# Kernel tuning notes

Measured on AMD Instinct MI355X. Metric: run time of the kernel, lower is better.

Reference implementation:

```python
import jax, jax.numpy as jnp
import numpy as np

EPS = 1e-5
NUM_GROUPS = 32
NUM_HEADS = 8

def group_norm(x, w, b):
    # x: (B, C, H, W), 32 groups, affine per-channel
    B, C, H, W = x.shape
    xg = x.reshape(B, NUM_GROUPS, C // NUM_GROUPS, H, W)
    mu = xg.mean(axis=(2, 3, 4), keepdims=True)
    var = xg.var(axis=(2, 3, 4), keepdims=True)
    xn = ((xg - mu) * jax.lax.rsqrt(var + EPS)).reshape(B, C, H, W)
    return xn * w[None, :, None, None] + b[None, :, None, None]

def conv1x1(x, w, b):
    # 1x1 conv == per-pixel linear; w: (out, in), x: (B, C, H, W)
    return jnp.einsum('oc,bchw->bohw', w, x) + b[None, :, None, None]

def setup_inputs() -> dict:
    key = jax.random.key(0)
    ks = jax.random.split(key, 4)
    B, C, H, W = 2, 512, 64, 64
    s = 1.0 / np.sqrt(C)
    return {
        'x': jax.random.normal(ks[0], (B, C, H, W), jnp.float32),
        'gn_w': jnp.ones((C,), jnp.float32),
        'gn_b': jnp.zeros((C,), jnp.float32),
        'wq': jax.random.normal(ks[1], (C, C), jnp.float32) * s,
        'bq': jnp.zeros((C,), jnp.float32),
        'wkv': jax.random.normal(ks[2], (2 * C, C), jnp.float32) * s,
        'bkv': jnp.zeros((2 * C,), jnp.float32),
        'wo': jax.random.normal(ks[3], (C, C), jnp.float32) * s,
        'bo': jnp.zeros((C,), jnp.float32),
    }

def reference(x, gn_w, gn_b, wq, bq, wkv, bkv, wo, bo):
    B, C, H, W = x.shape
    hd = C // NUM_HEADS  # head_dim
    residual = x
    x_norm = group_norm(x, gn_w, gn_b)
    q = conv1x1(x_norm, wq, bq).reshape(B, NUM_HEADS, hd, H * W)
    kv = conv1x1(x_norm, wkv, bkv)
    k, v = jnp.split(kv, 2, axis=1)
    k = k.reshape(B, NUM_HEADS, hd, H * W)
    v = v.reshape(B, NUM_HEADS, hd, H * W)
    scale = hd ** (-0.5)
    attn = jnp.einsum('bhdi,bhdj->bhij', q, k) * scale
    attn = jax.nn.softmax(attn, axis=-1)
    out = jnp.einsum('bhij,bhdj->bhdi', attn, v).reshape(B, C, H, W)
    out = conv1x1(out, wo, bo)
    return out + residual
```

## Files before the change

kernel.cpp:

```cpp
#include <hip/hip_runtime.h>
#include <cmath>

typedef __bf16 bf16x8 __attribute__((ext_vector_type(8)));
typedef __bf16 bf16x4 __attribute__((ext_vector_type(4)));
typedef float  f32x4  __attribute__((ext_vector_type(4)));
typedef unsigned uint2_ev __attribute__((ext_vector_type(2)));

static __device__ __forceinline__ f32x4 mfma16(bf16x8 a, bf16x8 b, f32x4 c) {
    return __builtin_amdgcn_mfma_f32_16x16x32_bf16(a, b, c, 0, 0, 0);
}

static __device__ __forceinline__ float fast_exp2(float x) {
#if __has_builtin(__builtin_amdgcn_exp2f)
    return __builtin_amdgcn_exp2f(x);
#else
    return exp2f(x);
#endif
}

static __device__ __forceinline__ void quad_swap(unsigned &a, unsigned &b) {
#if __has_builtin(__builtin_amdgcn_permlane32_swap) && __has_builtin(__builtin_amdgcn_permlane16_swap)
    uint2_ev r32 = __builtin_amdgcn_permlane32_swap(a, b, false, false);
    uint2_ev r16 = __builtin_amdgcn_permlane16_swap(r32[0], r32[1], false, false);
    a = r16[0]; b = r16[1];
#else
    asm volatile("v_permlane32_swap_b32 %0, %1\n\t"
                 "v_permlane16_swap_b32 %0, %1"
                 : "+v"(a), "+v"(b));
#endif
}

static __device__ __forceinline__ void gload_lds16(const void* g, void* l) {
    __builtin_amdgcn_global_load_lds((const __attribute__((address_space(1))) void*)g,
                                     (__attribute__((address_space(3))) void*)l, 16, 0, 0);
}

#define OFF_STATS 0
#define OFF_BEFF  1024
#define OFF_W     16384
#define OFF_XNT   (4u*1024*1024)
#define OFF_QKT   (OFF_XNT + 8u*1024*1024)
#define OFF_V     (OFF_QKT + 16u*1024*1024)
#define OFF_OP    (OFF_V + 8u*1024*1024)
#define CHUNK_O   4194304u
#define CHUNK_L   65536u

__global__ __launch_bounds__(256) void gn_fuse(const float* __restrict__ x,
                                               float* __restrict__ stats,
                                               __bf16* __restrict__ xT) {
    int p0 = blockIdx.x * 64, c0 = blockIdx.y * 64, b = blockIdx.z;
    int tid = threadIdx.x, lane = tid & 63, wave = tid >> 6;
    __shared__ float t[64][68];
    __shared__ float red[4][8];
    float acc_s[4] = {0.f,0.f,0.f,0.f}, acc_ss[4] = {0.f,0.f,0.f,0.f};
    const int rr = tid >> 4;
    const int p4 = (tid & 15) * 4;
    #pragma unroll
    for (int i = 0; i < 4; ++i) {
        int cc = rr + 16*i;
        float4 v = *(const float4*)&x[((size_t)(b*512 + c0 + cc) << 12) + p0 + p4];
        *(float4*)&t[cc][p4] = v;
        acc_s[i]  += v.x + v.y + v.z + v.w;
        acc_ss[i] += v.x*v.x + v.y*v.y + v.z*v.z + v.w*v.w;
    }
    #pragma unroll
    for (int g = 0; g < 4; ++g) {
        #pragma unroll
        for (int off = 1; off < 64; off <<= 1) {
            acc_s[g]  += __shfl_xor(acc_s[g],  off);
            acc_ss[g] += __shfl_xor(acc_ss[g], off);
        }
    }
    if (lane == 0) {
        #pragma unroll
        for (int g = 0; g < 4; ++g) { red[wave][g*2] = acc_s[g]; red[wave][g*2+1] = acc_ss[g]; }
    }
    __syncthreads();
    if (tid < 8) {
        float v0 = red[0][tid] + red[1][tid] + red[2][tid] + red[3][tid];
        int g = (b << 5) + (c0 >> 4) + (tid >> 1);
        atomicAdd(&stats[g*2 + (tid & 1)], v0);
    }
    const int ch = tid & 7;
    #pragma unroll
    for (int w = 0; w < 2; ++w) {
        int pp = (tid >> 3) + 32*w;
        __bf16 ob[8];
        #pragma unroll
        for (int e = 0; e < 8; ++e) ob[e] = (__bf16)t[ch*8 + e][pp];
        *(bf16x8*)&xT[((size_t)(b*4096 + p0 + pp) << 9) + c0 + ch*8] = *(bf16x8*)ob;
    }
}

__global__ __launch_bounds__(256) void prep_w(const float* __restrict__ wq,
                                              const float* __restrict__ wkv,
                                              const float* __restrict__ wo,
                                              const float* __restrict__ bq,
                                              const float* __restrict__ bkv,
                                              const float* __restrict__ stats,
                                              const float* __restrict__ gw,
                                              const float* __restrict__ gb,
                                              __bf16* __restrict__ wS,
                                              __bf16* __restrict__ wo_bf,
                                              float* __restrict__ beff) {
    const int b = blockIdx.y, bx = blockIdx.x;
    const int tid = threadIdx.x, lane = tid & 63, wave = tid >> 6;
    if (bx >= 48) {
        if (b) return;
        int r0 = (bx - 48) * 32;
        #pragma unroll
        for (int ps = 0; ps < 8; ++ps) {
            int row = r0 + ps*4 + wave;
            __bf16 obuf[8];
            #pragma unroll
            for (int e = 0; e < 8; ++e) obuf[e] = (__bf16)wo[(size_t)row*512 + lane*8 + e];
            *(bf16x8*)&wo_bf[(size_t)row*512 + lane*8] = *(bf16x8*)obuf;
        }
        return;
    }
    __shared__ float sS[512], sT[512];
    for (int c = tid; c < 512; c += 256) {
        int g = (b << 5) + (c >> 4);
        float mu   = stats[g*2] * (1.f/65536.f);
        float var  = stats[g*2+1] * (1.f/65536.f) - mu*mu;
        float rstd = rsqrtf(var + 1e-5f);
        float s = rstd * gw[c];
        sS[c] = s;
        sT[c] = gb[c] - mu * s;
    }
    __syncthreads();
    int r0 = bx * 32;
    #pragma unroll
    for (int ps = 0; ps < 8; ++ps) {
        int row = r0 + ps*4 + wave;
        const float* Wrow = (row < 512) ? (wq + (size_t)row*512) : (wkv + (size_t)(row-512)*512);
        float bias0 = (row < 512) ? bq[row] : bkv[row - 512];
        float bp = 0.f;
        __bf16 obuf[8];
        #pragma unroll
        for (int e = 0; e < 8; ++e) {
            int c = lane*8 + e;
            float wv_ = Wrow[c];
            obuf[e] = (__bf16)(wv_ * sS[c]);
            bp += wv_ * sT[c];
        }
        *(bf16x8*)&wS[((size_t)b*1536 + row)*512 + lane*8] = *(bf16x8*)obuf;
        #pragma unroll
        for (int off = 1; off < 64; off <<= 1) bp += __shfl_xor(bp, off);
        if (lane == 0) beff[b*1536 + row] = bias0 + bp;
    }
}

__global__ __launch_bounds__(256) void gemm128_kernel(
    const __bf16* __restrict__ A, const __bf16* __restrict__ B,
    const float* __restrict__ bias, int nsplit,
    float scale0, void* __restrict__ out,
    int N, int K, long long strideA, long long strideB, long long strideO, int biasStride) {
    const int bz = blockIdx.z;
    A += strideA * bz;
    B += strideB * bz;
    const float* bb = bias + (size_t)bz * biasStride;
    const int m0 = blockIdx.x * 128, n0 = blockIdx.y * 128;
    const int tid = threadIdx.x, lane = tid & 63, wave = tid >> 6;
    const int quad = lane >> 4, l16 = lane & 15;
    const int wm = (wave >> 1) * 64, wn = (wave & 1) * 64;

    __shared__ __attribute__((aligned(16))) __bf16 lds_a[2][128][64];
    __shared__ __attribute__((aligned(16))) __bf16 lds_b[2][128][64];

    f32x4 acc[4][4];
    #pragma unroll
    for (int mt = 0; mt < 4; ++mt)
        #pragma unroll
        for (int nt = 0; nt < 4; ++nt)
            #pragma unroll
            for (int r = 0; r < 4; ++r) acc[mt][nt][r] = 0.f;

    const int myrow = (wave << 3) + (lane >> 3);
    const int mych  = ((lane & 7) ^ (myrow & 7)) << 3;
    const __bf16* Ab = A + (size_t)(m0 + myrow) * K + mych;
    const __bf16* Bb = B + (size_t)(n0 + myrow) * K + mych;

    auto stage = [&](int buf, int kt) {
        char* la = (char*)(&lds_a[buf][0][0]) + (wave << 10);
        char* lb = (char*)(&lds_b[buf][0][0]) + (wave << 10);
        #pragma unroll
        for (int i = 0; i < 4; ++i) {
            gload_lds16(Ab + kt + (size_t)(32*i) * K, la + i*4096);
            gload_lds16(Bb + kt + (size_t)(32*i) * K, lb + i*4096);
        }
    };

    stage(0, 0);
    const int NK = K >> 6;
    for (int k8 = 0; k8 < NK; ++k8) {
        __syncthreads();
        const int cur = k8 & 1;
        if (k8 + 1 < NK) stage(cur ^ 1, (k8 + 1) << 6);
        #pragma unroll
        for (int kh = 0; kh < 2; ++kh) {
            bf16x8 af[4], bfr[4];
            #pragma unroll
            for (int mt = 0; mt < 4; ++mt)
                af[mt] = *(const bf16x8*)&lds_a[cur][wm + mt*16 + l16][(((kh<<2)|quad) ^ (l16 & 7)) * 8];
            #pragma unroll
            for (int nt = 0; nt < 4; ++nt)
                bfr[nt] = *(const bf16x8*)&lds_b[cur][wn + nt*16 + l16][(((kh<<2)|quad) ^ (l16 & 7)) * 8];
            #pragma unroll
            for (int mt = 0; mt < 4; ++mt)
                #pragma unroll
                for (int nt = 0; nt < 4; ++nt)
                    acc[mt][nt] = mfma16(af[mt], bfr[nt], acc[mt][nt]);
        }
    }

    #pragma unroll
    for (int mt = 0; mt < 4; ++mt) {
        const int mrow = m0 + wm + mt*16 + quad*4;
        #pragma unroll
        for (int nt = 0; nt < 4; ++nt) {
            const int ncol = n0 + wn + nt*16 + l16;
            #pragma unroll
            for (int r = 0; r < 4; ++r) {
                const int m = mrow + r;
                float val = acc[mt][nt][r] + bb[ncol];
                if (ncol < nsplit) val *= scale0;
                ((__bf16*)out)[(size_t)strideO * bz + (size_t)m * N + ncol] = (__bf16)val;
            }
        }
    }
}

template<int OUT_F32, int HAS_RES>
__global__ __launch_bounds__(256) void gemm64_kernel(
    const __bf16* __restrict__ A, const __bf16* __restrict__ B,
    const float* __restrict__ bias, const float* __restrict__ res,
    void* __restrict__ out,
    int N, int K, long long strideA, long long strideB, long long strideO, int biasStride) {
    const int bz = blockIdx.z;
    A += strideA * bz;
    B += strideB * bz;
    const float* bb = bias + (size_t)bz * biasStride;
    const int m0 = blockIdx.x * 64, n0 = blockIdx.y * 128;
    const int tid = threadIdx.x, lane = tid & 63, wave = tid >> 6;
    const int quad = lane >> 4, l16 = lane & 15;
    const int wn = wave * 32;

    __shared__ __attribute__((aligned(16))) __bf16 lds_a[2][64][64];
    __shared__ __attribute__((aligned(16))) __bf16 lds_b[2][128][64];

    f32x4 acc[4][2];
    #pragma unroll
    for (int mt = 0; mt < 4; ++mt)
        #pragma unroll
        for (int nt = 0; nt < 2; ++nt)
            #pragma unroll
            for (int r = 0; r < 4; ++r) acc[mt][nt][r] = 0.f;

    const int myrow = (wave << 3) + (lane >> 3);
    const int mych  = ((lane & 7) ^ (myrow & 7)) << 3;
    const __bf16* Ab = A + (size_t)(m0 + myrow) * K + mych;
    const __bf16* Bb = B + (size_t)(n0 + myrow) * K + mych;

    auto stage = [&](int buf, int kt) {
        char* la = (char*)(&lds_a[buf][0][0]) + (wave << 10);
        char* lb = (char*)(&lds_b[buf][0][0]) + (wave << 10);
        #pragma unroll
        for (int i = 0; i < 2; ++i)
            gload_lds16(Ab + kt + (size_t)(32*i) * K, la + i*4096);
        #pragma unroll
        for (int i = 0; i < 4; ++i)
            gload_lds16(Bb + kt + (size_t)(32*i) * K, lb + i*4096);
    };

    stage(0, 0);
    const int NK = K >> 6;
    for (int k8 = 0; k8 < NK; ++k8) {
        __syncthreads();
        const int cur = k8 & 1;
        if (k8 + 1 < NK) stage(cur ^ 1, (k8 + 1) << 6);
        #pragma unroll
        for (int kh = 0; kh < 2; ++kh) {
            bf16x8 af[4], bfr[2];
            #pragma unroll
            for (int mt = 0; mt < 4; ++mt)
                af[mt] = *(const bf16x8*)&lds_a[cur][mt*16 + l16][(((kh<<2)|quad) ^ (l16 & 7)) * 8];
            #pragma unroll
            for (int nt = 0; nt < 2; ++nt)
                bfr[nt] = *(const bf16x8*)&lds_b[cur][wn + nt*16 + l16][(((kh<<2)|quad) ^ (l16 & 7)) * 8];
            #pragma unroll
            for (int mt = 0; mt < 4; ++mt)
                #pragma unroll
                for (int nt = 0; nt < 2; ++nt)
                    acc[mt][nt] = mfma16(af[mt], bfr[nt], acc[mt][nt]);
        }
    }

    #pragma unroll
    for (int mt = 0; mt < 4; ++mt) {
        const int mrow = m0 + mt*16 + quad*4;
        #pragma unroll
        for (int nt = 0; nt < 2; ++nt) {
            const int ncol = n0 + wn + nt*16 + l16;
            #pragma unroll
            for (int r = 0; r < 4; ++r) {
                const int m = mrow + r;
                float val = acc[mt][nt][r] + bb[m];
                const size_t idx = (size_t)strideO * bz + (size_t)m * N + ncol;
                if constexpr (HAS_RES) val += res[idx];
                if constexpr (OUT_F32) ((float*)out)[idx] = val;
                else ((__bf16*)out)[idx] = (__bf16)val;
            }
        }
    }
}

template<int NCH>
__global__ __launch_bounds__(256, 3) void attn_kernel(const __bf16* __restrict__ qkT,
                                                      const __bf16* __restrict__ v,
                                                      __bf16* __restrict__ attnT,
                                                      __bf16* __restrict__ Opart,
                                                      float* __restrict__ Lpart) {
    const int b = blockIdx.y >> 3, h = blockIdx.y & 7;
    const int chunk = (NCH > 1) ? blockIdx.z : 0;
    int NITER, kt0;
    if constexpr (NCH == 3) {
        NITER = (chunk == 0) ? 22 : 21;
        kt0   = (chunk == 0) ? 0 : (chunk == 1 ? 1408 : 2752);
    } else {
        NITER = 64 / NCH;
        kt0   = chunk * (4096 / NCH);
    }
    const int tid = threadIdx.x;
    const int wave = tid >> 6, lane = tid & 63;
    const int quad = lane >> 4, l16 = lane & 15;
    const int qbase = blockIdx.x * 256 + wave * 64;

    const __bf16* qkTb = qkT + ((size_t)b << 22);
    const __bf16* vb   = v   + ((size_t)b << 21);

    __shared__ __attribute__((aligned(16))) __bf16 lds_k[2][64][64];
    __shared__ __attribute__((aligned(16))) __bf16 lds_v[2][64][64];

    bf16x8 aq[4][2];
    #pragma unroll
    for (int mt = 0; mt < 4; ++mt) {
        const __bf16* qrow = qkTb + (size_t)(qbase + mt*16 + l16) * 1024 + h*64 + quad*8;
        aq[mt][0] = *(const bf16x8*)qrow;
        aq[mt][1] = *(const bf16x8*)(qrow + 32);
    }
    f32x4 o[4][5];
    #pragma unroll
    for (int mt = 0; mt < 4; ++mt)
        #pragma unroll
        for (int dt = 0; dt < 5; ++dt)
            #pragma unroll
            for (int r = 0; r < 4; ++r) o[mt][dt][r] = 0.f;
    const f32x4 kZero = {0.f, 0.f, 0.f, 0.f};

    bf16x8 onesb;
    #pragma unroll
    for (int e = 0; e < 8; ++e) onesb[e] = (__bf16)1.0f;

    const int myrow = (wave << 3) + (lane >> 3);
    const int mych  = ((lane & 7) ^ (myrow & 7)) << 3;
    const __bf16* kgb = qkTb + (size_t)myrow * 1024 + 512 + h*64 + mych;
    const __bf16* vgb = vb + ((size_t)(h*64 + myrow) << 12) + mych;

    auto stage = [&](int buf, int kt) {
        char* kb = (char*)(&lds_k[buf][0][0]) + (wave << 10);
        char* vp = (char*)(&lds_v[buf][0][0]) + (wave << 10);
        const __bf16* kg = kgb + (size_t)kt * 1024;
        const __bf16* vg = vgb + kt;
        gload_lds16(kg,                       kb);
        gload_lds16(kg + 32*1024,             kb + 4096);
        gload_lds16(vg,                       vp);
        gload_lds16(vg + ((size_t)32 << 12),  vp + 4096);
    };

    stage(0, kt0);

    for (int it = 0; it < NITER; ++it) {
        __syncthreads();
        const int cur = it & 1;
        if (it + 1 < NITER) stage(cur ^ 1, kt0 + (it + 1) * 64);

        #pragma unroll
        for (int kh = 0; kh < 2; ++kh) {
            __builtin_amdgcn_s_setprio(1);
            unsigned pd[4][4];
            #pragma unroll
            for (int j = 0; j < 2; ++j) {
                const int nt = kh*2 + j;
                const int kr = nt*16 + l16;
                bf16x8 bk0 = *(const bf16x8*)&lds_k[cur][kr][( quad      ^ (l16 & 7)) * 8];
                bf16x8 bk1 = *(const bf16x8*)&lds_k[cur][kr][((4 + quad) ^ (l16 & 7)) * 8];
                #pragma unroll
                for (int mt = 0; mt < 4; ++mt) {
                    f32x4 s = mfma16(bk1, aq[mt][1], mfma16(bk0, aq[mt][0], kZero));
                    f32x4 p;
                    #pragma unroll
                    for (int r = 0; r < 4; ++r) p[r] = fast_exp2(s[r]);
                    bf16x4 pb = __builtin_convertvector(p, bf16x4);
                    union { bf16x4 v; unsigned d[2]; } u; u.v = pb;
                    pd[mt][j*2]     = u.d[0];
                    pd[mt][j*2 + 1] = u.d[1];
                }
            }
            bf16x8 pa[4];
            #pragma unroll
            for (int mt = 0; mt < 4; ++mt) {
                unsigned x0 = pd[mt][0], x1 = pd[mt][1];
                unsigned y0 = pd[mt][2], y1 = pd[mt][3];
                quad_swap(x0, y0);
                quad_swap(x1, y1);
                union { unsigned d[4]; bf16x8 v; } u;
                u.d[0] = x0; u.d[1] = x1; u.d[2] = y0; u.d[3] = y1;
                pa[mt] = u.v;
            }
            #pragma unroll
            for (int dt = 0; dt < 4; ++dt) {
                bf16x8 bv = *(const bf16x8*)&lds_v[cur][dt*16 + l16][((kh*4 + quad) ^ (l16 & 7)) * 8];
                #pragma unroll
                for (int mt = 0; mt < 4; ++mt)
                    o[mt][dt] = mfma16(pa[mt], bv, o[mt][dt]);
            }
            #pragma unroll
            for (int mt = 0; mt < 4; ++mt)
                o[mt][4] = mfma16(pa[mt], onesb, o[mt][4]);
            __builtin_amdgcn_s_setprio(0);
        }
    }

    if constexpr (NCH > 1) {
        __bf16* Ob = Opart + (size_t)chunk * CHUNK_O;
        #pragma unroll
        for (int mt = 0; mt < 4; ++mt)
            #pragma unroll
            for (int dt = 0; dt < 4; ++dt)
                #pragma unroll
                for (int r = 0; r < 4; ++r) {
                    size_t row = (size_t)b * 4096 + qbase + mt*16 + quad*4 + r;
                    Ob[(row << 9) + (h << 6) + dt*16 + l16] = (__bf16)o[mt][dt][r];
                }
        if (l16 == 0) {
            #pragma unroll
            for (int mt = 0; mt < 4; ++mt)
                #pragma unroll
                for (int r = 0; r < 4; ++r) {
                    int p = qbase + mt*16 + quad*4 + r;
                    Lpart[(size_t)chunk * CHUNK_L + (size_t)(((b*8 + h)) << 12) + p] = o[mt][4][r];
                }
        }
    } else {
        #pragma unroll
        for (int mt = 0; mt < 4; ++mt) {
            float inv[4];
            #pragma unroll
            for (int r = 0; r < 4; ++r)
                inv[r] = 1.f / __shfl(o[mt][4][r], lane & 48);
            #pragma unroll
            for (int dt = 0; dt < 4; ++dt)
                #pragma unroll
                for (int r = 0; r < 4; ++r) {
                    size_t row = (size_t)b * 4096 + qbase + mt*16 + quad*4 + r;
                    attnT[(row << 9) + (h << 6) + dt*16 + l16] = (__bf16)(o[mt][dt][r] * inv[r]);
                }
        }
    }
}

template<int NCH>
__global__ __launch_bounds__(256) void attn_combine(const __bf16* __restrict__ Opart,
                                                    const float* __restrict__ Lpart,
                                                    __bf16* __restrict__ attnT) {
    int i = blockIdx.x * 256 + threadIdx.x;
    int c8 = i & 63;
    int p  = (i >> 6) & 4095;
    int b  = i >> 18;
    int h  = c8 >> 3;
    size_t lidx = (size_t)((b*8 + h) << 12) + p;
    float l = 0.f;
    #pragma unroll
    for (int ch = 0; ch < NCH; ++ch) l += Lpart[(size_t)ch * CHUNK_L + lidx];
    float inv = 1.f / l;
    size_t oi = ((size_t)(b*4096 + p) << 9) + c8*8;
    float acc[8] = {0.f,0.f,0.f,0.f,0.f,0.f,0.f,0.f};
    #pragma unroll
    for (int ch = 0; ch < NCH; ++ch) {
        bf16x8 ov = *(const bf16x8*)&Opart[(size_t)ch * CHUNK_O + oi];
        #pragma unroll
        for (int r = 0; r < 8; ++r) acc[r] += (float)ov[r];
    }
    bf16x8 rv;
    #pragma unroll
    for (int r = 0; r < 8; ++r) rv[r] = (__bf16)(acc[r] * inv);
    *(bf16x8*)&attnT[oi] = rv;
}

extern "C" void kernel_launch(void* const* d_in, const int* in_sizes, int n_in,
                              void* d_out, int out_size, void* d_ws, size_t ws_size,
                              hipStream_t stream) {
    const float* x   = (const float*)d_in[0];
    const float* gnw = (const float*)d_in[1];
    const float* gnb = (const float*)d_in[2];
    const float* wq  = (const float*)d_in[3];
    const float* bq  = (const float*)d_in[4];
    const float* wkv = (const float*)d_in[5];
    const float* bkv = (const float*)d_in[6];
    const float* wo  = (const float*)d_in[7];
    const float* bo  = (const float*)d_in[8];
    float* out = (float*)d_out;

    char* ws = (char*)d_ws;
    float*  stats  = (float*)(ws + OFF_STATS);
    float*  beff   = (float*)(ws + OFF_BEFF);
    __bf16* wS     = (__bf16*)(ws + OFF_W);
    __bf16* wo_bf  = wS + 2u*1536*512;
    __bf16* xT     = (__bf16*)(ws + OFF_XNT);
    __bf16* qkT    = (__bf16*)(ws + OFF_QKT);
    __bf16* vv     = (__bf16*)(ws + OFF_V);
    __bf16* Opart  = (__bf16*)(ws + OFF_OP);
    __bf16* attnT  = xT;

    const size_t need3 = (size_t)OFF_OP + 3u * (CHUNK_O * 2 + CHUNK_L * 4);
    const size_t need2 = (size_t)OFF_OP + 2u * (CHUNK_O * 2 + CHUNK_L * 4);
    const int nch = (ws_size >= need3) ? 3 : (ws_size >= need2 ? 2 : 1);
    float* Lpart = (float*)(ws + OFF_OP + (size_t)nch * CHUNK_O * 2);

    hipMemsetAsync(stats, 0, 512, stream);
    gn_fuse<<<dim3(64, 8, 2), 256, 0, stream>>>(x, stats, xT);
    prep_w<<<dim3(64, 2), 256, 0, stream>>>(wq, wkv, wo, bq, bkv, stats, gnw, gnb,
                                            wS, wo_bf, beff);

    const long long S  = 2097152LL;
    const long long S2 = 4194304LL;
    const long long SW = 1536LL*512;
    gemm128_kernel<<<dim3(32, 8, 2), 256, 0, stream>>>(
        xT, wS, beff, 512, 0.125f * 1.44269504f, qkT, 1024, 512, S, SW, S2, 1536);
    gemm64_kernel<0,0><<<dim3(8, 32, 2), 256, 0, stream>>>(
        wS + 1024*512, xT, beff + 1024, nullptr, vv, 4096, 512, SW, S, S, 1536);

    if (nch == 3) {
        attn_kernel<3><<<dim3(16, 16, 3), 256, 0, stream>>>(qkT, vv, nullptr, Opart, Lpart);
        attn_combine<3><<<2048, 256, 0, stream>>>(Opart, Lpart, attnT);
    } else if (nch == 2) {
        attn_kernel<2><<<dim3(16, 16, 2), 256, 0, stream>>>(qkT, vv, nullptr, Opart, Lpart);
        attn_combine<2><<<2048, 256, 0, stream>>>(Opart, Lpart, attnT);
    } else {
        attn_kernel<1><<<dim3(16, 16, 1), 256, 0, stream>>>(qkT, vv, attnT, nullptr, nullptr);
    }

    gemm64_kernel<1,1><<<dim3(8, 32, 2), 256, 0, stream>>>(
        wo_bf, attnT, bo, x, out, 4096, 512, 0, S, S, 0);
}
```

Before: 214.0 us.

## Fuse attention split-combine into output projection GEMM B-operand loading

Removes the separate attn_combine kernel and instead sums the partial attention outputs and normalizes by the summed softmax denominators while staging the B tile of the output-projection GEMM. This avoids a launch and the write/read round trip of the combined attention tensor. In exchange, B staging switches from direct global-to-LDS loads to register loads plus arithmetic and LDS stores, and each m-block re-reads all chunk partials.

```diff
diff --git a/kernel.cpp b/kernel.cpp
--- a/kernel.cpp
+++ b/kernel.cpp
@@ -231,10 +231,11 @@
     }
 }
 
-template<int OUT_F32, int HAS_RES>
+template<int OUT_F32, int HAS_RES, int COMB>
 __global__ __launch_bounds__(256) void gemm64_kernel(
     const __bf16* __restrict__ A, const __bf16* __restrict__ B,
     const float* __restrict__ bias, const float* __restrict__ res,
+    const float* __restrict__ Lp,
     void* __restrict__ out,
     int N, int K, long long strideA, long long strideB, long long strideO, int biasStride) {
     const int bz = blockIdx.z;
@@ -262,23 +263,71 @@
     const __bf16* Ab = A + (size_t)(m0 + myrow) * K + mych;
     const __bf16* Bb = B + (size_t)(n0 + myrow) * K + mych;
 
-    auto stage = [&](int buf, int kt) {
+    auto stageA = [&](int buf, int kt) {
         char* la = (char*)(&lds_a[buf][0][0]) + (wave << 10);
-        char* lb = (char*)(&lds_b[buf][0][0]) + (wave << 10);
         #pragma unroll
         for (int i = 0; i < 2; ++i)
             gload_lds16(Ab + kt + (size_t)(32*i) * K, la + i*4096);
+    };
+    auto stageB_dma = [&](int buf, int kt) {
+        char* lb = (char*)(&lds_b[buf][0][0]) + (wave << 10);
         #pragma unroll
         for (int i = 0; i < 4; ++i)
             gload_lds16(Bb + kt + (size_t)(32*i) * K, lb + i*4096);
     };
 
-    stage(0, 0);
+    bf16x8 brq[4][COMB ? COMB : 1];
+    float  lq [4][COMB ? COMB : 1];
+    auto loadB = [&](int kt) {
+        if constexpr (COMB) {
+            const int h = kt >> 6;
+            #pragma unroll
+            for (int i = 0; i < 4; ++i) {
+                const int p = n0 + myrow + 32*i;
+                const size_t bi = (((size_t)bz*4096 + p) << 9) + kt + mych;
+                const size_t li = ((size_t)((bz*8 + h)) << 12) + p;
+                #pragma unroll
+                for (int ch = 0; ch < COMB; ++ch) {
+                    brq[i][ch] = *(const bf16x8*)&B[(size_t)ch * CHUNK_O + bi];
+                    lq[i][ch]  = Lp[(size_t)ch * CHUNK_L + li];
+                }
+            }
+        }
+    };
+    auto writeB = [&](int buf) {
+        if constexpr (COMB) {
+            #pragma unroll
+            for (int i = 0; i < 4; ++i) {
+                float l = 0.f;
+                #pragma unroll
+                for (int ch = 0; ch < COMB; ++ch) l += lq[i][ch];
+                float inv = 1.f / l;
+                __bf16 ob[8];
+                #pragma unroll
+                for (int e = 0; e < 8; ++e) {
+                    float a = 0.f;
+                    #pragma unroll
+                    for (int ch = 0; ch < COMB; ++ch) a += (float)brq[i][ch][e];
+                    ob[e] = (__bf16)(a * inv);
+                }
+                *(bf16x8*)&lds_b[buf][myrow + 32*i][(lane & 7) * 8] = *(bf16x8*)ob;
+            }
+        }
+    };
+
+    stageA(0, 0);
+    if constexpr (COMB) { loadB(0); writeB(0); }
+    else stageB_dma(0, 0);
+
     const int NK = K >> 6;
     for (int k8 = 0; k8 < NK; ++k8) {
         __syncthreads();
         const int cur = k8 & 1;
-        if (k8 + 1 < NK) stage(cur ^ 1, (k8 + 1) << 6);
+        if (k8 + 1 < NK) {
+            stageA(cur ^ 1, (k8 + 1) << 6);
+            if constexpr (COMB) loadB((k8 + 1) << 6);
+            else stageB_dma(cur ^ 1, (k8 + 1) << 6);
+        }
         #pragma unroll
         for (int kh = 0; kh < 2; ++kh) {
             bf16x8 af[4], bfr[2];
@@ -294,6 +343,7 @@
                 for (int nt = 0; nt < 2; ++nt)
                     acc[mt][nt] = mfma16(af[mt], bfr[nt], acc[mt][nt]);
         }
+        if constexpr (COMB) { if (k8 + 1 < NK) writeB(cur ^ 1); }
     }
 
     #pragma unroll
@@ -470,34 +520,6 @@
     }
 }
 
-template<int NCH>
-__global__ __launch_bounds__(256) void attn_combine(const __bf16* __restrict__ Opart,
-                                                    const float* __restrict__ Lpart,
-                                                    __bf16* __restrict__ attnT) {
-    int i = blockIdx.x * 256 + threadIdx.x;
-    int c8 = i & 63;
-    int p  = (i >> 6) & 4095;
-    int b  = i >> 18;
-    int h  = c8 >> 3;
-    size_t lidx = (size_t)((b*8 + h) << 12) + p;
-    float l = 0.f;
-    #pragma unroll
-    for (int ch = 0; ch < NCH; ++ch) l += Lpart[(size_t)ch * CHUNK_L + lidx];
-    float inv = 1.f / l;
-    size_t oi = ((size_t)(b*4096 + p) << 9) + c8*8;
-    float acc[8] = {0.f,0.f,0.f,0.f,0.f,0.f,0.f,0.f};
-    #pragma unroll
-    for (int ch = 0; ch < NCH; ++ch) {
-        bf16x8 ov = *(const bf16x8*)&Opart[(size_t)ch * CHUNK_O + oi];
-        #pragma unroll
-        for (int r = 0; r < 8; ++r) acc[r] += (float)ov[r];
-    }
-    bf16x8 rv;
-    #pragma unroll
-    for (int r = 0; r < 8; ++r) rv[r] = (__bf16)(acc[r] * inv);
-    *(bf16x8*)&attnT[oi] = rv;
-}
-
 extern "C" void kernel_launch(void* const* d_in, const int* in_sizes, int n_in,
                               void* d_out, int out_size, void* d_ws, size_t ws_size,
                               hipStream_t stream) {
@@ -538,19 +560,20 @@
     const long long SW = 1536LL*512;
     gemm128_kernel<<<dim3(32, 8, 2), 256, 0, stream>>>(
         xT, wS, beff, 512, 0.125f * 1.44269504f, qkT, 1024, 512, S, SW, S2, 1536);
-    gemm64_kernel<0,0><<<dim3(8, 32, 2), 256, 0, stream>>>(
-        wS + 1024*512, xT, beff + 1024, nullptr, vv, 4096, 512, SW, S, S, 1536);
+    gemm64_kernel<0,0,0><<<dim3(8, 32, 2), 256, 0, stream>>>(
+        wS + 1024*512, xT, beff + 1024, nullptr, nullptr, vv, 4096, 512, SW, S, S, 1536);
 
     if (nch == 3) {
         attn_kernel<3><<<dim3(16, 16, 3), 256, 0, stream>>>(qkT, vv, nullptr, Opart, Lpart);
-        attn_combine<3><<<2048, 256, 0, stream>>>(Opart, Lpart, attnT);
+        gemm64_kernel<1,1,3><<<dim3(8, 32, 2), 256, 0, stream>>>(
+            wo_bf, Opart, bo, x, Lpart, out, 4096, 512, 0, 0, S, 0);
     } else if (nch == 2) {
         attn_kernel<2><<<dim3(16, 16, 2), 256, 0, stream>>>(qkT, vv, nullptr, Opart, Lpart);
-        attn_combine<2><<<2048, 256, 0, stream>>>(Opart, Lpart, attnT);
+        gemm64_kernel<1,1,2><<<dim3(8, 32, 2), 256, 0, stream>>>(
+            wo_bf, Opart, bo, x, Lpart, out, 4096, 512, 0, 0, S, 0);
     } else {
         attn_kernel<1><<<dim3(16, 16, 1), 256, 0, stream>>>(qkT, vv, attnT, nullptr, nullptr);
-    }
-
-    gemm64_kernel<1,1><<<dim3(8, 32, 2), 256, 0, stream>>>(
-        wo_bf, attnT, bo, x, out, 4096, 512, 0, S, S, 0);
-}
+        gemm64_kernel<1,1,0><<<dim3(8, 32, 2), 256, 0, stream>>>(
+            wo_bf, attnT, bo, x, nullptr, out, 4096, 512, 0, S, S, 0);
+    }
+}
```

Measured after the change: 223.4 us. 4.4% more time.
